# Kernel optimization log

Measured on AMD Instinct MI355X. Metric: run time of the kernel, lower is better.

## Reference

```python
import jax, jax.numpy as jnp
import numpy as np

Q = 4          # num_quantizers
K = 2048       # codebook_size
D = 256        # dim
B, N = 8, 8192 # batch, tokens (N % Q == 0)


def l2norm(t, eps=1e-12):
    return t / jnp.maximum(jnp.linalg.norm(t, axis=-1, keepdims=True), eps)


def setup_inputs() -> dict:
    key = jax.random.key(0)
    kx, ke = jax.random.split(key)
    x = jax.random.normal(kx, (B, N, D), dtype=jnp.float32)
    embed = jax.random.normal(ke, (Q, K, D), dtype=jnp.float32)
    return {"x": x, "embed": embed}


def reference(x, embed):
    b, n, d = x.shape
    q = embed.shape[0]
    m = n // q  # tokens per quantizer chunk
    # chunk along token axis (dim=1), as torch.chunk(x, Q, dim=1)
    xc = x.reshape(b, q, m, d).transpose(1, 0, 2, 3)  # [Q, B, M, D]

    def one_vq(xq, eq):
        # xq: [B, M, D], eq: [K, D]
        xn = l2norm(xq)
        en = l2norm(eq)
        dist = jnp.einsum('bmd,kd->bmk', xn, en)   # cosine similarity
        ind = jnp.argmax(dist, axis=-1)            # temp=0 gumbel -> argmax
        quant = eq[ind]                            # F.embedding with raw embed
        return quant, ind

    quant_c, ind_c = jax.vmap(one_vq)(xc, embed)   # [Q,B,M,D], [Q,B,M]
    quantized = quant_c.transpose(1, 0, 2, 3).reshape(b, n, d)
    encoding = ind_c.transpose(1, 0, 2).reshape(b, n)
    # eval mode: loss is sum of Q zero tensors of shape [1]
    vq_loss = jnp.zeros((1,), dtype=x.dtype)
    return quantized, encoding, vq_loss
```

## Files before the change

### kernel.cpp

```cpp
#include <hip/hip_runtime.h>
#include <math.h>

#define Bq 8
#define Nq 8192
#define Dq 256
#define Qq 4
#define Kq 2048
#define Mq (Nq / Qq)
#define TT (Bq * Nq)
#define QUANT_ELEMS ((size_t)TT * Dq)

#define CAP1Q 4096
#define THRESH 3e-4f

#define WS_CNT_OFF    0u
#define WS_LIST_OFF   1024u
#define WS_SX_OFF     66560u
#define WS_PSC_OFF    328704u
#define WS_PCD_OFF    852992u
#define WS_ENH_OFF    1377280u
#define WS_ENP_OFF    5571584u
#define WS_PART_OFF   13960192u

typedef __attribute__((ext_vector_type(8))) _Float16 f16x8;
typedef __attribute__((ext_vector_type(4))) _Float16 f16x4;
typedef __attribute__((ext_vector_type(4))) float    f32x4;

__device__ __forceinline__ void async_load16(const void* g, void* s) {
    __builtin_amdgcn_global_load_lds(
        (const __attribute__((address_space(1))) void*)g,
        (__attribute__((address_space(3))) void*)s, 16, 0, 0);
}

__device__ __forceinline__ float f32_div(float a, float b) {
    return (float)((double)a / (double)b);
}

__device__ __forceinline__ float np_norm_wave(const float* __restrict__ src, int ln) {
#pragma clang fp contract(off)
    float r = 0.0f;
    if (ln < 16) {
        const float* p = src + (ln >> 3) * 128 + (ln & 7);
        #pragma unroll
        for (int m = 0; m < 16; ++m) { float v = p[m * 8]; r = r + v * v; }
    }
    float t = r + __shfl_xor(r, 1, 64);
    t = t + __shfl_xor(t, 2, 64);
    t = t + __shfl_xor(t, 4, 64);
    float b0 = __shfl(t, 0, 64);
    float b1 = __shfl(t, 8, 64);
    float n2 = b0 + b1;
    return fmaxf((float)sqrt((double)n2), 1e-12f);
}

__global__ __launch_bounds__(256) void prep_kernel(const float* __restrict__ embed,
                                                   const float* __restrict__ x,
                                                   char* __restrict__ enh,
                                                   float* __restrict__ enp,
                                                   float* __restrict__ sxa,
                                                   int* __restrict__ cnt,
                                                   float* __restrict__ out) {
    if (blockIdx.x >= 2048) {
        const int tid = threadIdx.x;
        const int qd  = tid & 3;
        const int row = (blockIdx.x - 2048) * 64 + (tid >> 2);
        const float* xr = x + (size_t)row * Dq + qd * 8;
        float s2 = 0.f;
        #pragma unroll
        for (int ch = 0; ch < 8; ++ch) {
            float4 u = *(const float4*)(xr + ch * 32);
            float4 v = *(const float4*)(xr + ch * 32 + 4);
            s2 += u.x * u.x + u.y * u.y + u.z * u.z + u.w * u.w;
            s2 += v.x * v.x + v.y * v.y + v.z * v.z + v.w * v.w;
        }
        s2 += __shfl_xor(s2, 1, 64);
        s2 += __shfl_xor(s2, 2, 64);
        float sxv = 1.0f / fmaxf(sqrtf(s2), 1e-12f);
        if (qd == 0) sxa[row] = sxv;
        return;
    }

    if (blockIdx.x == 0) {
        if (threadIdx.x < 4) cnt[threadIdx.x] = 0;
        if (threadIdx.x == 0) out[QUANT_ELEMS + TT] = 0.0f;
    }

    int row = blockIdx.x * 4 + (threadIdx.x >> 6);
    int ln  = threadIdx.x & 63;
    const float* src = embed + (size_t)row * Dq;

    float4 v = *(const float4*)(src + ln * 4);
    float s = v.x * v.x + v.y * v.y + v.z * v.z + v.w * v.w;
    #pragma unroll
    for (int m = 1; m < 64; m <<= 1) s += __shfl_xor(s, m, 64);
    float sx = 1.0f / fmaxf(sqrtf(s), 1e-12f);
    int q = row >> 11, k = row & 2047, Tb = k >> 5, c = k & 31;
    int g = ln >> 1, h = ln & 1;
    f16x4 o;
    o[0] = (_Float16)(v.x * sx); o[1] = (_Float16)(v.y * sx);
    o[2] = (_Float16)(v.z * sx); o[3] = (_Float16)(v.w * sx);
    char* dst = enh + ((size_t)(q * 64 + Tb)) * 16384 + c * 512 + ((g ^ c) << 4) + h * 8;
    *(f16x4*)dst = o;

    float nm = np_norm_wave(src, ln);
    float* dstp = enp + (size_t)row * Dq;
    #pragma unroll
    for (int e = 0; e < 4; ++e) dstp[ln * 4 + e] = f32_div(src[ln * 4 + e], nm);
}

__global__ __launch_bounds__(256, 2) void gemm_kernel(const float* __restrict__ x,
                                                      const float* __restrict__ sxa,
                                                      const char* __restrict__ enh,
                                                      float4* __restrict__ part) {
    __shared__ __align__(16) char es[2][16384];

    const int tid = threadIdx.x;
    const int wv  = tid >> 6;
    const int ln  = tid & 63;
    const int qd  = ln >> 4;
    const int l15 = ln & 15;

    const int bid = blockIdx.x;
    const int h   = bid & 1;
    const int g   = bid >> 1;
    const int b   = g >> 5;
    const int rem = g & 31;
    const int q   = rem >> 3;
    const int m0  = (rem & 7) << 8;
    const int t0  = b * Nq + q * Mq + m0;
    const int t0w = t0 + wv * 64;

    f16x8 ah[4][8];
    #pragma unroll
    for (int mf = 0; mf < 4; ++mf) {
        const int tok = t0w + mf * 16 + l15;
        const float sxv = sxa[tok];
        const float* xr = x + (size_t)tok * Dq + qd * 8;
        #pragma unroll
        for (int ch = 0; ch < 8; ++ch) {
            float4 u = *(const float4*)(xr + ch * 32);
            float4 v = *(const float4*)(xr + ch * 32 + 4);
            f16x8 f;
            f[0] = (_Float16)(u.x * sxv); f[1] = (_Float16)(u.y * sxv);
            f[2] = (_Float16)(u.z * sxv); f[3] = (_Float16)(u.w * sxv);
            f[4] = (_Float16)(v.x * sxv); f[5] = (_Float16)(v.y * sxv);
            f[6] = (_Float16)(v.z * sxv); f[7] = (_Float16)(v.w * sxv);
            ah[mf][ch] = f;
        }
    }

    float b1[4][4], b2[4][4];
    int   ic[4][4];
    #pragma unroll
    for (int mf = 0; mf < 4; ++mf)
        #pragma unroll
        for (int r = 0; r < 4; ++r) { b1[mf][r] = -2.0f; b2[mf][r] = -2.0f; ic[mf][r] = 0; }

    const char* ebase = enh + ((size_t)(q * 64 + h * 32)) * 16384;

    #pragma unroll
    for (int i = 0; i < 4; ++i) {
        int off = i * 4096 + wv * 1024 + ln * 16;
        async_load16(ebase + off, es[0] + off);
    }
    __syncthreads();

    for (int T = 0; T < 32; ++T) {
        if (T + 1 < 32) {
            const char* src = ebase + (size_t)(T + 1) * 16384;
            #pragma unroll
            for (int i = 0; i < 4; ++i) {
                int off = i * 4096 + wv * 1024 + ln * 16;
                async_load16(src + off, es[(T + 1) & 1] + off);
            }
        }
        const char* esb = es[T & 1];

        #pragma unroll
        for (int s = 0; s < 2; ++s) {
            const int  c  = s * 16 + l15;
            const char* cb = esb + c * 512;
            f16x8 bfr[8];
            #pragma unroll
            for (int ch = 0; ch < 8; ++ch)
                bfr[ch] = *(const f16x8*)(cb + ((((ch << 2) | qd) ^ c) << 4));

            f32x4 a[4];
            #pragma unroll
            for (int mf = 0; mf < 4; ++mf) a[mf] = (f32x4){0.f, 0.f, 0.f, 0.f};
            #pragma unroll
            for (int ch = 0; ch < 8; ++ch) {
                #pragma unroll
                for (int mf = 0; mf < 4; ++mf)
                    a[mf] = __builtin_amdgcn_mfma_f32_16x16x32_f16(ah[mf][ch], bfr[ch], a[mf], 0, 0, 0);
            }

            const int cg = (h << 10) | (T << 5) | (s << 4) | l15;
            #pragma unroll
            for (int mf = 0; mf < 4; ++mf)
                #pragma unroll
                for (int r = 0; r < 4; ++r) {
                    float sv = a[mf][r];
                    bool  gt = sv > b1[mf][r];
                    b2[mf][r] = __builtin_amdgcn_fmed3f(sv, b1[mf][r], b2[mf][r]);
                    b1[mf][r] = fmaxf(b1[mf][r], sv);
                    ic[mf][r] = gt ? cg : ic[mf][r];
                }
        }
        __syncthreads();
    }

    float fb1[4][4], fb2[4][4];
    int   fic[4][4];
    #pragma unroll
    for (int mf = 0; mf < 4; ++mf)
        #pragma unroll
        for (int r = 0; r < 4; ++r) {
            float v1 = b1[mf][r], v2 = b2[mf][r]; int vi = ic[mf][r];
            #pragma unroll
            for (int m = 1; m < 16; m <<= 1) {
                float o1 = __shfl_xor(v1, m, 64);
                float o2 = __shfl_xor(v2, m, 64);
                int   oi = __shfl_xor(vi, m, 64);
                if (o1 > v1 || (o1 == v1 && oi < vi)) { v2 = fmaxf(v1, o2); v1 = o1; vi = oi; }
                else v2 = fmaxf(v2, o1);
            }
            fb1[mf][r] = v1; fb2[mf][r] = v2; fic[mf][r] = vi;
        }

    if (l15 == 0) {
        #pragma unroll
        for (int mf = 0; mf < 4; ++mf)
            #pragma unroll
            for (int r = 0; r < 4; ++r) {
                int t = t0w + mf * 16 + qd * 4 + r;
                float4 pv;
                pv.x = fb1[mf][r];
                pv.y = fb2[mf][r];
                pv.z = __int_as_float(fic[mf][r]);
                pv.w = 0.f;
                part[(size_t)h * TT + t] = pv;
            }
    }
}

__global__ __launch_bounds__(256) void merge_kernel(const float* __restrict__ embed,
                                                    const float4* __restrict__ part,
                                                    float* __restrict__ out,
                                                    int* __restrict__ cnt,
                                                    int* __restrict__ list) {
    const int wv = threadIdx.x >> 6, ln = threadIdx.x & 63;
    const int nw = gridDim.x * 4;

    for (int t = blockIdx.x * 4 + wv; t < TT; t += nw) {
        float4 pa = part[t];
        float4 pb = part[TT + t];
        float v1, v2; int vi;
        if (pb.x > pa.x) { v1 = pb.x; vi = __float_as_int(pb.z); v2 = fmaxf(pa.x, pb.y); }
        else             { v1 = pa.x; vi = __float_as_int(pa.z); v2 = fmaxf(pb.x, pa.y); }
        const int q = (t >> 11) & 3;

        if (ln == 0) {
            out[QUANT_ELEMS + (size_t)t] = (float)vi;
            if (v1 - v2 < THRESH) {
                int pos = atomicAdd(&cnt[q], 1);
                if (pos < CAP1Q) list[q * CAP1Q + pos] = t;
            }
        }
        const float* er = embed + ((size_t)(q * Kq + vi)) * Dq;
        float4 v = *(const float4*)(er + ln * 4);
        *(float4*)(out + (size_t)t * Dq + ln * 4) = v;
    }
}

__global__ __launch_bounds__(256) void fix_partial(const float* __restrict__ x,
                                                   const float* __restrict__ enp,
                                                   const int* __restrict__ cnt,
                                                   const int* __restrict__ list,
                                                   float* __restrict__ pscore,
                                                   int* __restrict__ pcode) {
#pragma clang fp contract(off)
    __shared__ float xn[16][Dq];
    __shared__ int   stok[16];
    __shared__ float wp_s[4][16];
    __shared__ int   wp_c[4][16];

    const int tid = threadIdx.x;
    const int wv  = tid >> 6;
    const int ln  = tid & 63;

    int cq[4], nbq[4], total = 0;
    #pragma unroll
    for (int q = 0; q < 4; ++q) {
        int c = cnt[q]; if (c > CAP1Q) c = CAP1Q;
        cq[q] = c; nbq[q] = (c + 15) >> 4; total += nbq[q] * 8;
    }

    for (int j = blockIdx.x; j < total; j += gridDim.x) {
        int rem = j, q = 0;
        while (rem >= nbq[q] * 8) { rem -= nbq[q] * 8; ++q; }
        const int batch = rem >> 3, chunk = rem & 7;

        if (tid < 16) {
            int idx = batch * 16 + tid;
            stok[tid] = list[q * CAP1Q + (idx < cq[q] ? idx : batch * 16)];
        }
        __syncthreads();
        for (int r = 0; r < 4; ++r) {
            int i = wv * 4 + r;
            const float* xr = x + (size_t)stok[i] * Dq;
            float nm = np_norm_wave(xr, ln);
            #pragma unroll
            for (int e = 0; e < 4; ++e)
                xn[i][ln * 4 + e] = f32_div(xr[ln * 4 + e], nm);
        }
        __syncthreads();

        const int c = chunk * 256 + tid;
        const float* er = enp + ((size_t)(q * Kq + c)) * Dq;
        float l0[16], l1[16], l2[16], l3[16];
        #pragma unroll
        for (int i = 0; i < 16; ++i) { l0[i] = 0.f; l1[i] = 0.f; l2[i] = 0.f; l3[i] = 0.f; }

        for (int d = 0; d < Dq; d += 4) {
            float4 e = *(const float4*)(er + d);
            #pragma unroll
            for (int i = 0; i < 16; ++i) {
                float4 xv = *(const float4*)&xn[i][d];
                l0[i] = l0[i] + xv.x * e.x;
                l1[i] = l1[i] + xv.y * e.y;
                l2[i] = l2[i] + xv.z * e.z;
                l3[i] = l3[i] + xv.w * e.w;
            }
        }

        #pragma unroll
        for (int i = 0; i < 16; ++i) {
            float s = (l0[i] + l1[i]) + (l2[i] + l3[i]);
            int bc = c;
            #pragma unroll
            for (int m = 1; m < 64; m <<= 1) {
                float os = __shfl_xor(s, m, 64);
                int   oc = __shfl_xor(bc, m, 64);
                if (os > s || (os == s && oc < bc)) { s = os; bc = oc; }
            }
            if (ln == 0) { wp_s[wv][i] = s; wp_c[wv][i] = bc; }
        }
        __syncthreads();
        if (tid < 16) {
            int idx = batch * 16 + tid;
            if (idx < cq[q]) {
                float s = wp_s[0][tid]; int bc = wp_c[0][tid];
                #pragma unroll
                for (int w2 = 1; w2 < 4; ++w2) {
                    float os = wp_s[w2][tid]; int oc = wp_c[w2][tid];
                    if (os > s || (os == s && oc < bc)) { s = os; bc = oc; }
                }
                int p = q * CAP1Q + idx;
                pscore[p * 8 + chunk] = s;
                pcode[p * 8 + chunk]  = bc;
            }
        }
        __syncthreads();
    }
}

__global__ __launch_bounds__(256) void fix_final(const float* __restrict__ embed,
                                                 const int* __restrict__ cnt,
                                                 const int* __restrict__ list,
                                                 const float* __restrict__ pscore,
                                                 const int* __restrict__ pcode,
                                                 float* __restrict__ out) {
    int cq[4], tot = 0;
    #pragma unroll
    for (int q = 0; q < 4; ++q) {
        int c = cnt[q]; if (c > CAP1Q) c = CAP1Q;
        cq[q] = c; tot += c;
    }
    const int wv = threadIdx.x >> 6, ln = threadIdx.x & 63;

    for (int j = blockIdx.x * 4 + wv; j < tot; j += gridDim.x * 4) {
        int rem = j, q = 0;
        while (rem >= cq[q]) { rem -= cq[q]; ++q; }
        int p = q * CAP1Q + rem;
        int t = list[p];
        int bc = 0;
        if (ln == 0) {
            float bs = pscore[p * 8]; bc = pcode[p * 8];
            #pragma unroll
            for (int ch = 1; ch < 8; ++ch) {
                float s = pscore[p * 8 + ch]; int c2 = pcode[p * 8 + ch];
                if (s > bs || (s == bs && c2 < bc)) { bs = s; bc = c2; }
            }
            out[QUANT_ELEMS + (size_t)t] = (float)bc;
        }
        bc = __shfl(bc, 0, 64);
        const float* er = embed + ((size_t)(q * Kq + bc)) * Dq;
        float4 v = *(const float4*)(er + ln * 4);
        *(float4*)(out + (size_t)t * Dq + ln * 4) = v;
    }
}

extern "C" void kernel_launch(void* const* d_in, const int* in_sizes, int n_in,
                              void* d_out, int out_size, void* d_ws, size_t ws_size,
                              hipStream_t stream) {
    const float* x     = (const float*)d_in[0];
    const float* embed = (const float*)d_in[1];
    float* out = (float*)d_out;
    char*  ws  = (char*)d_ws;
    int*    cnt    = (int*)(ws + WS_CNT_OFF);
    int*    list   = (int*)(ws + WS_LIST_OFF);
    float*  sxa    = (float*)(ws + WS_SX_OFF);
    float*  pscore = (float*)(ws + WS_PSC_OFF);
    int*    pcode  = (int*)(ws + WS_PCD_OFF);
    char*   enh    = ws + WS_ENH_OFF;
    float*  enp    = (float*)(ws + WS_ENP_OFF);
    float4* part   = (float4*)(ws + WS_PART_OFF);

    prep_kernel<<<3072, 256, 0, stream>>>(embed, x, enh, enp, sxa, cnt, out);
    gemm_kernel<<<512, 256, 0, stream>>>(x, sxa, enh, part);
    merge_kernel<<<2048, 256, 0, stream>>>(embed, part, out, cnt, list);
    fix_partial<<<1024, 256, 0, stream>>>(x, enp, cnt, list, pscore, pcode);
    fix_final<<<256, 256, 0, stream>>>(embed, cnt, list, pscore, pcode, out);
}
```

Before: 295.3 us.

## Replace exhaustive fp32 fixup with fp16 MFMA candidate filter plus exact rescoring

The old fixup scored every ambiguous token against all 2048 codes in exact fp32 across two kernels. The new single kernel rescans the codebook with fp16 MFMA, keeping only codes within a threshold of the best approximate score, then rescores just those candidates in fp32 and writes the index and embedding directly. This cuts the fp32 work and removes one launch and the partial-result buffers. In exchange it repeats a full fp16 GEMM pass over ambiguous tokens, serializes per-token rescoring with many block barriers, and falls back to a full scan when more than 16 candidates survive.

```diff
diff --git a/kernel.cpp b/kernel.cpp
--- a/kernel.cpp
+++ b/kernel.cpp
@@ -12,6 +12,7 @@
 
 #define CAP1Q 4096
 #define THRESH 3e-4f
+#define CAND_MAX 16
 
 #define WS_CNT_OFF    0u
 #define WS_LIST_OFF   1024u
@@ -273,131 +274,171 @@
     }
 }
 
-__global__ __launch_bounds__(256) void fix_partial(const float* __restrict__ x,
+__global__ __launch_bounds__(256) void cand_kernel(const float* __restrict__ x,
+                                                   const float* __restrict__ sxa,
+                                                   const char* __restrict__ enh,
                                                    const float* __restrict__ enp,
+                                                   const float4* __restrict__ part,
+                                                   const float* __restrict__ embed,
                                                    const int* __restrict__ cnt,
                                                    const int* __restrict__ list,
-                                                   float* __restrict__ pscore,
-                                                   int* __restrict__ pcode) {
+                                                   float* __restrict__ out) {
 #pragma clang fp contract(off)
-    __shared__ float xn[16][Dq];
-    __shared__ int   stok[16];
-    __shared__ float wp_s[4][16];
-    __shared__ int   wp_c[4][16];
+    __shared__ __align__(16) char es[2][16384];
+    __shared__ int   stok[64];
+    __shared__ float sv1[64];
+    __shared__ int   scnt[64];
+    __shared__ unsigned short scand[64][CAND_MAX];
 
     const int tid = threadIdx.x;
     const int wv  = tid >> 6;
     const int ln  = tid & 63;
+    const int qd  = ln >> 4;
+    const int l15 = ln & 15;
 
     int cq[4], nbq[4], total = 0;
     #pragma unroll
     for (int q = 0; q < 4; ++q) {
         int c = cnt[q]; if (c > CAP1Q) c = CAP1Q;
-        cq[q] = c; nbq[q] = (c + 15) >> 4; total += nbq[q] * 8;
+        cq[q] = c; nbq[q] = (c + 63) >> 6; total += nbq[q];
     }
 
     for (int j = blockIdx.x; j < total; j += gridDim.x) {
         int rem = j, q = 0;
-        while (rem >= nbq[q] * 8) { rem -= nbq[q] * 8; ++q; }
-        const int batch = rem >> 3, chunk = rem & 7;
-
-        if (tid < 16) {
-            int idx = batch * 16 + tid;
-            stok[tid] = list[q * CAP1Q + (idx < cq[q] ? idx : batch * 16)];
+        while (rem >= nbq[q]) { rem -= nbq[q]; ++q; }
+        const int base = rem << 6;
+
+        if (tid < 64) {
+            int idx = base + tid;
+            int tok = list[q * CAP1Q + (idx < cq[q] ? idx : base)];
+            stok[tid] = tok;
+            scnt[tid] = 0;
+            sv1[tid]  = fmaxf(part[tok].x, part[TT + tok].x);
         }
         __syncthreads();
-        for (int r = 0; r < 4; ++r) {
-            int i = wv * 4 + r;
-            const float* xr = x + (size_t)stok[i] * Dq;
+
+        f16x8 ah[8];
+        {
+            const int tok = stok[wv * 16 + l15];
+            const float sxv = sxa[tok];
+            const float* xr = x + (size_t)tok * Dq + qd * 8;
+            #pragma unroll
+            for (int ch = 0; ch < 8; ++ch) {
+                float4 u = *(const float4*)(xr + ch * 32);
+                float4 v = *(const float4*)(xr + ch * 32 + 4);
+                f16x8 f;
+                f[0] = (_Float16)(u.x * sxv); f[1] = (_Float16)(u.y * sxv);
+                f[2] = (_Float16)(u.z * sxv); f[3] = (_Float16)(u.w * sxv);
+                f[4] = (_Float16)(v.x * sxv); f[5] = (_Float16)(v.y * sxv);
+                f[6] = (_Float16)(v.z * sxv); f[7] = (_Float16)(v.w * sxv);
+                ah[ch] = f;
+            }
+        }
+        float thr[4];
+        #pragma unroll
+        for (int r = 0; r < 4; ++r) thr[r] = sv1[wv * 16 + qd * 4 + r] - THRESH;
+
+        const char* ebase = enh + ((size_t)(q * 64)) * 16384;
+        #pragma unroll
+        for (int i = 0; i < 4; ++i) {
+            int off = i * 4096 + wv * 1024 + ln * 16;
+            async_load16(ebase + off, es[0] + off);
+        }
+        __syncthreads();
+
+        for (int T = 0; T < 64; ++T) {
+            if (T + 1 < 64) {
+                const char* src = ebase + (size_t)(T + 1) * 16384;
+                #pragma unroll
+                for (int i = 0; i < 4; ++i) {
+                    int off = i * 4096 + wv * 1024 + ln * 16;
+                    async_load16(src + off, es[(T + 1) & 1] + off);
+                }
+            }
+            const char* esb = es[T & 1];
+
+            #pragma unroll
+            for (int s = 0; s < 2; ++s) {
+                const int  c  = s * 16 + l15;
+                const char* cb = esb + c * 512;
+                f16x8 bfr[8];
+                #pragma unroll
+                for (int ch = 0; ch < 8; ++ch)
+                    bfr[ch] = *(const f16x8*)(cb + ((((ch << 2) | qd) ^ c) << 4));
+
+                f32x4 a = {0.f, 0.f, 0.f, 0.f};
+                #pragma unroll
+                for (int ch = 0; ch < 8; ++ch)
+                    a = __builtin_amdgcn_mfma_f32_16x16x32_f16(ah[ch], bfr[ch], a, 0, 0, 0);
+
+                const int cg = (T << 5) | (s << 4) | l15;
+                #pragma unroll
+                for (int r = 0; r < 4; ++r) {
+                    if (a[r] >= thr[r]) {
+                        int slot = wv * 16 + qd * 4 + r;
+                        int pos = atomicAdd(&scnt[slot], 1);
+                        if (pos < CAND_MAX) scand[slot][pos] = (unsigned short)cg;
+                    }
+                }
+            }
+            __syncthreads();
+        }
+
+        float* xnw = (float*)(es[0] + wv * 4096);
+        for (int i = 0; i < 16; ++i) {
+            const int slot = wv * 16 + i;
+            const int tok  = stok[slot];
+            const float* xr = x + (size_t)tok * Dq;
             float nm = np_norm_wave(xr, ln);
             #pragma unroll
             for (int e = 0; e < 4; ++e)
-                xn[i][ln * 4 + e] = f32_div(xr[ln * 4 + e], nm);
+                xnw[ln * 4 + e] = f32_div(xr[ln * 4 + e], nm);
+            __syncthreads();
+
+            const int ncand = scnt[slot];
+            float bs = -2.0f; int bc = 0x7fffffff;
+            if (ncand <= CAND_MAX) {
+                if (ln < ncand) {
+                    int code = scand[slot][ln];
+                    const float* er2 = enp + ((size_t)(q * Kq + code)) * Dq;
+                    float l0 = 0.f, l1 = 0.f, l2 = 0.f, l3 = 0.f;
+                    for (int d = 0; d < Dq; d += 4) {
+                        float4 e = *(const float4*)(er2 + d);
+                        float4 xv = *(const float4*)&xnw[d];
+                        l0 = l0 + xv.x * e.x; l1 = l1 + xv.y * e.y;
+                        l2 = l2 + xv.z * e.z; l3 = l3 + xv.w * e.w;
+                    }
+                    bs = (l0 + l1) + (l2 + l3);
+                    bc = code;
+                }
+            } else {
+                for (int k = 0; k < 32; ++k) {
+                    int code = k * 64 + ln;
+                    const float* er2 = enp + ((size_t)(q * Kq + code)) * Dq;
+                    float l0 = 0.f, l1 = 0.f, l2 = 0.f, l3 = 0.f;
+                    for (int d = 0; d < Dq; d += 4) {
+                        float4 e = *(const float4*)(er2 + d);
+                        float4 xv = *(const float4*)&xnw[d];
+                        l0 = l0 + xv.x * e.x; l1 = l1 + xv.y * e.y;
+                        l2 = l2 + xv.z * e.z; l3 = l3 + xv.w * e.w;
+                    }
+                    float sE = (l0 + l1) + (l2 + l3);
+                    if (sE > bs || (sE == bs && code < bc)) { bs = sE; bc = code; }
+                }
+            }
+            #pragma unroll
+            for (int m = 1; m < 64; m <<= 1) {
+                float os = __shfl_xor(bs, m, 64);
+                int   oc = __shfl_xor(bc, m, 64);
+                if (os > bs || (os == bs && oc < bc)) { bs = os; bc = oc; }
+            }
+            if (ln == 0) out[QUANT_ELEMS + (size_t)tok] = (float)bc;
+            const float* er = embed + ((size_t)(q * Kq + bc)) * Dq;
+            float4 v = *(const float4*)(er + ln * 4);
+            *(float4*)(out + (size_t)tok * Dq + ln * 4) = v;
+            __syncthreads();
         }
         __syncthreads();
-
-        const int c = chunk * 256 + tid;
-        const float* er = enp + ((size_t)(q * Kq + c)) * Dq;
-        float l0[16], l1[16], l2[16], l3[16];
-        #pragma unroll
-        for (int i = 0; i < 16; ++i) { l0[i] = 0.f; l1[i] = 0.f; l2[i] = 0.f; l3[i] = 0.f; }
-
-        for (int d = 0; d < Dq; d += 4) {
-            float4 e = *(const float4*)(er + d);
-            #pragma unroll
-            for (int i = 0; i < 16; ++i) {
-                float4 xv = *(const float4*)&xn[i][d];
-                l0[i] = l0[i] + xv.x * e.x;
-                l1[i] = l1[i] + xv.y * e.y;
-                l2[i] = l2[i] + xv.z * e.z;
-                l3[i] = l3[i] + xv.w * e.w;
-            }
-        }
-
-        #pragma unroll
-        for (int i = 0; i < 16; ++i) {
-            float s = (l0[i] + l1[i]) + (l2[i] + l3[i]);
-            int bc = c;
-            #pragma unroll
-            for (int m = 1; m < 64; m <<= 1) {
-                float os = __shfl_xor(s, m, 64);
-                int   oc = __shfl_xor(bc, m, 64);
-                if (os > s || (os == s && oc < bc)) { s = os; bc = oc; }
-            }
-            if (ln == 0) { wp_s[wv][i] = s; wp_c[wv][i] = bc; }
-        }
-        __syncthreads();
-        if (tid < 16) {
-            int idx = batch * 16 + tid;
-            if (idx < cq[q]) {
-                float s = wp_s[0][tid]; int bc = wp_c[0][tid];
-                #pragma unroll
-                for (int w2 = 1; w2 < 4; ++w2) {
-                    float os = wp_s[w2][tid]; int oc = wp_c[w2][tid];
-                    if (os > s || (os == s && oc < bc)) { s = os; bc = oc; }
-                }
-                int p = q * CAP1Q + idx;
-                pscore[p * 8 + chunk] = s;
-                pcode[p * 8 + chunk]  = bc;
-            }
-        }
-        __syncthreads();
-    }
-}
-
-__global__ __launch_bounds__(256) void fix_final(const float* __restrict__ embed,
-                                                 const int* __restrict__ cnt,
-                                                 const int* __restrict__ list,
-                                                 const float* __restrict__ pscore,
-                                                 const int* __restrict__ pcode,
-                                                 float* __restrict__ out) {
-    int cq[4], tot = 0;
-    #pragma unroll
-    for (int q = 0; q < 4; ++q) {
-        int c = cnt[q]; if (c > CAP1Q) c = CAP1Q;
-        cq[q] = c; tot += c;
-    }
-    const int wv = threadIdx.x >> 6, ln = threadIdx.x & 63;
-
-    for (int j = blockIdx.x * 4 + wv; j < tot; j += gridDim.x * 4) {
-        int rem = j, q = 0;
-        while (rem >= cq[q]) { rem -= cq[q]; ++q; }
-        int p = q * CAP1Q + rem;
-        int t = list[p];
-        int bc = 0;
-        if (ln == 0) {
-            float bs = pscore[p * 8]; bc = pcode[p * 8];
-            #pragma unroll
-            for (int ch = 1; ch < 8; ++ch) {
-                float s = pscore[p * 8 + ch]; int c2 = pcode[p * 8 + ch];
-                if (s > bs || (s == bs && c2 < bc)) { bs = s; bc = c2; }
-            }
-            out[QUANT_ELEMS + (size_t)t] = (float)bc;
-        }
-        bc = __shfl(bc, 0, 64);
-        const float* er = embed + ((size_t)(q * Kq + bc)) * Dq;
-        float4 v = *(const float4*)(er + ln * 4);
-        *(float4*)(out + (size_t)t * Dq + ln * 4) = v;
     }
 }
 
@@ -411,8 +452,6 @@
     int*    cnt    = (int*)(ws + WS_CNT_OFF);
     int*    list   = (int*)(ws + WS_LIST_OFF);
     float*  sxa    = (float*)(ws + WS_SX_OFF);
-    float*  pscore = (float*)(ws + WS_PSC_OFF);
-    int*    pcode  = (int*)(ws + WS_PCD_OFF);
     char*   enh    = ws + WS_ENH_OFF;
     float*  enp    = (float*)(ws + WS_ENP_OFF);
     float4* part   = (float4*)(ws + WS_PART_OFF);
@@ -420,6 +459,5 @@
     prep_kernel<<<3072, 256, 0, stream>>>(embed, x, enh, enp, sxa, cnt, out);
     gemm_kernel<<<512, 256, 0, stream>>>(x, sxa, enh, part);
     merge_kernel<<<2048, 256, 0, stream>>>(embed, part, out, cnt, list);
-    fix_partial<<<1024, 256, 0, stream>>>(x, enp, cnt, list, pscore, pcode);
-    fix_final<<<256, 256, 0, stream>>>(embed, cnt, list, pscore, pcode, out);
-}
+    cand_kernel<<<256, 256, 0, stream>>>(x, sxa, enh, enp, part, embed, cnt, list, out);
+}
```

Result: slower. 393.9 us (+33.4%).
